# Kernel tuning notes

Measured on AMD Instinct MI355X. Metric: run time of the kernel, lower is better.

Reference implementation:

```python
import jax, jax.numpy as jnp
import numpy as np

B, S, D = 2, 2048, 768
H = 12
DK = D // H  # 64; dim_q = dim_k = dim_v
DFF = 3072
EPS = 1e-5


def layer_norm(x, w, b):
    mu = jnp.mean(x, axis=-1, keepdims=True)
    var = jnp.var(x, axis=-1, keepdims=True)
    return (x - mu) * jax.lax.rsqrt(var + EPS) * w + b


def setup_inputs() -> dict:
    key = jax.random.key(0)
    ks = jax.random.split(key, 12)
    s = 0.02
    return {
        "src": jax.random.normal(ks[0], (B, S, D), dtype=jnp.float32),
        # per-head projections stacked over heads: [H, D, DK]
        "Wq": jax.random.normal(ks[1], (H, D, DK), dtype=jnp.float32) * s,
        "bq": jnp.zeros((H, DK), dtype=jnp.float32),
        "Wk": jax.random.normal(ks[2], (H, D, DK), dtype=jnp.float32) * s,
        "bk": jnp.zeros((H, DK), dtype=jnp.float32),
        "Wv": jax.random.normal(ks[3], (H, D, DK), dtype=jnp.float32) * s,
        "bv": jnp.zeros((H, DK), dtype=jnp.float32),
        # output projection: [H*DK, D]
        "Wo": jax.random.normal(ks[4], (H * DK, D), dtype=jnp.float32) * s,
        "bo": jnp.zeros((D,), dtype=jnp.float32),
        "ln1_w": jnp.ones((D,), dtype=jnp.float32),
        "ln1_b": jnp.zeros((D,), dtype=jnp.float32),
        "W1": jax.random.normal(ks[5], (D, DFF), dtype=jnp.float32) * s,
        "b1": jnp.zeros((DFF,), dtype=jnp.float32),
        "W2": jax.random.normal(ks[6], (DFF, D), dtype=jnp.float32) * s,
        "b2": jnp.zeros((D,), dtype=jnp.float32),
        "ln2_w": jnp.ones((D,), dtype=jnp.float32),
        "ln2_b": jnp.zeros((D,), dtype=jnp.float32),
    }


def reference(src, Wq, bq, Wk, bk, Wv, bv, Wo, bo, ln1_w, ln1_b,
              W1, b1, W2, b2, ln2_w, ln2_b):
    # per-head q/k/v projections, batched over heads via einsum
    q = jnp.einsum('bsd,hdk->bhsk', src, Wq) + bq[None, :, None, :]
    k = jnp.einsum('bsd,hdk->bhsk', src, Wk) + bk[None, :, None, :]
    v = jnp.einsum('bsd,hdk->bhsk', src, Wv) + bv[None, :, None, :]
    scale = jnp.asarray(DK, src.dtype) ** 0.5
    scores = jnp.einsum('bhsk,bhtk->bhst', q, k) / scale  # [B,H,S,S]
    attn = jax.nn.softmax(scores, axis=-1)
    ctx = jnp.einsum('bhst,bhtk->bhsk', attn, v)
    # concat heads along feature dim (matches torch.cat over head outputs)
    ctx = ctx.transpose(0, 2, 1, 3).reshape(src.shape[0], src.shape[1], H * DK)
    attn_out = ctx @ Wo + bo
    x = layer_norm(src + attn_out, ln1_w, ln1_b)
    ff = jax.nn.relu(x @ W1 + b1) @ W2 + b2
    return layer_norm(x + ff, ln2_w, ln2_b)
```

## Files before the change

### kernel.cpp

```cpp
#include <hip/hip_runtime.h>
#include <hip/hip_bf16.h>

#define S_LEN 2048
#define DMODEL 768
#define NHEAD 12
#define DKH 64
#define DFF_K 3072
#define MROWS 4096
#define KSPLIT 2
#define KHALF (S_LEN / KSPLIT)

typedef __attribute__((ext_vector_type(8))) short bf16x8;
typedef __attribute__((ext_vector_type(8))) unsigned short us8;
typedef __attribute__((ext_vector_type(4))) float f32x4;

__device__ __forceinline__ float bfu2f(unsigned short u) {
  return __uint_as_float(((unsigned int)u) << 16);
}
__device__ __forceinline__ unsigned short f2bfu(float f) {
  __hip_bfloat16 h = __float2bfloat16(f);
  return *reinterpret_cast<unsigned short*>(&h);
}

__global__ __launch_bounds__(256) void convert_kernel(
    const float* __restrict__ in, unsigned short* __restrict__ out, int n4)
{
  const int i = blockIdx.x * 256 + threadIdx.x;
  if (i < n4) {
    float4 v = *(const float4*)(in + (size_t)i * 4);
    ushort4 o;
    o.x = f2bfu(v.x); o.y = f2bfu(v.y); o.z = f2bfu(v.z); o.w = f2bfu(v.w);
    *(ushort4*)(out + (size_t)i * 4) = o;
  }
}

__device__ __forceinline__ void transpose_conv_body(
    const float* in, unsigned short* out, int R, int Ctot, int head,
    int bx, int by, int tid)
{
  __shared__ float t[64][68];
  const int r0 = bx * 64;
  const int c0 = by * 64;
  const float* ib;
  int ld;
  if (head) { ib = in + (size_t)by * R * 64; ld = 64; }
  else      { ib = in + c0;                  ld = Ctot; }
  const int lr = tid >> 4;
  const int lc = (tid & 15) << 2;

#pragma unroll
  for (int rr = 0; rr < 4; ++rr) {
    const int row = rr * 16 + lr;
    float4 v = *(const float4*)(ib + (size_t)(r0 + row) * ld + lc);
    t[row][lc + 0] = v.x; t[row][lc + 1] = v.y;
    t[row][lc + 2] = v.z; t[row][lc + 3] = v.w;
  }
  __syncthreads();
#pragma unroll
  for (int rr = 0; rr < 4; ++rr) {
    const int oc = rr * 16 + lr;
    ushort4 o;
    o.x = f2bfu(t[lc + 0][oc]); o.y = f2bfu(t[lc + 1][oc]);
    o.z = f2bfu(t[lc + 2][oc]); o.w = f2bfu(t[lc + 3][oc]);
    *(ushort4*)(out + (size_t)(c0 + oc) * R + r0 + lc) = o;
  }
}

__global__ __launch_bounds__(256) void transpose_conv_kernel(
    const float* __restrict__ in, unsigned short* __restrict__ out,
    int R, int Ctot, int head)
{
  transpose_conv_body(in, out, R, Ctot, head, blockIdx.x, blockIdx.y, threadIdx.x);
}

__global__ __launch_bounds__(256) void transpose_conv4_kernel(
    const float* __restrict__ i0, const float* __restrict__ i1,
    const float* __restrict__ i2, const float* __restrict__ i3,
    unsigned short* __restrict__ o0, unsigned short* __restrict__ o1,
    unsigned short* __restrict__ o2, unsigned short* __restrict__ o3)
{
  const int z = blockIdx.z;
  const float* in = (z == 0) ? i0 : (z == 1) ? i1 : (z == 2) ? i2 : i3;
  unsigned short* out = (z == 0) ? o0 : (z == 1) ? o1 : (z == 2) ? o2 : o3;
  transpose_conv_body(in, out, DMODEL, DMODEL, (z < 3) ? 1 : 0,
                      blockIdx.x, blockIdx.y, threadIdx.x);
}

template<int BN>
__global__ __launch_bounds__(256) void mfma_gemm_kernel(
    const unsigned short* __restrict__ A,
    const unsigned short* __restrict__ BT,
    const float* __restrict__ bias,
    unsigned short* __restrict__ C,
    int K, int N, int relu, int klen, size_t out_stride)
{
  constexpr int WN = (BN == 128) ? 64 : 32;
  constexpr int NJ = WN / 16;
  __shared__ unsigned short As[128][40];
  __shared__ unsigned short Bs[BN][40];

  const int tid  = threadIdx.x;
  const int wid  = tid >> 6;
  const int lane = tid & 63;
  const int ml   = lane & 15;
  const int quad = lane >> 4;
  const int wm   = (wid & 1) * 64;
  const int wn   = (wid >> 1) * WN;
  const int row0 = blockIdx.x * 128;
  const int col0 = blockIdx.y * BN;
  const int zed  = blockIdx.z;
  const int kb0  = zed * klen;
  const int kend = kb0 + klen;

  const int sr = tid >> 2;
  const int sk = (tid & 3) << 3;

  const unsigned short* pA0 = A  + (size_t)(row0 + sr) * K + sk;
  const unsigned short* pA1 = A  + (size_t)(row0 + sr + 64) * K + sk;
  const unsigned short* pB0 = BT + (size_t)(col0 + sr) * K + sk;
  const unsigned short* pB1 = BT + (size_t)(col0 + sr + 64) * K + sk;

  f32x4 acc[4][NJ];
#pragma unroll
  for (int i = 0; i < 4; ++i)
#pragma unroll
    for (int j = 0; j < NJ; ++j)
#pragma unroll
      for (int r = 0; r < 4; ++r) acc[i][j][r] = 0.f;

  us8 ra0 = *(const us8*)(pA0 + kb0);
  us8 ra1 = *(const us8*)(pA1 + kb0);
  us8 rb0 = *(const us8*)(pB0 + kb0);
  us8 rb1;
  if (BN == 128) rb1 = *(const us8*)(pB1 + kb0);

  for (int k0 = kb0; k0 < kend; k0 += 32) {
    *(us8*)&As[sr][sk]      = ra0;
    *(us8*)&As[sr + 64][sk] = ra1;
    *(us8*)&Bs[sr][sk]      = rb0;
    if (BN == 128) *(us8*)&Bs[sr + 64][sk] = rb1;
    __syncthreads();

    const int kn = k0 + 32;
    if (kn < kend) {
      ra0 = *(const us8*)(pA0 + kn);
      ra1 = *(const us8*)(pA1 + kn);
      rb0 = *(const us8*)(pB0 + kn);
      if (BN == 128) rb1 = *(const us8*)(pB1 + kn);
    }

    bf16x8 af[4], bfr[NJ];
#pragma unroll
    for (int i = 0; i < 4; ++i)
      af[i] = *(const bf16x8*)&As[wm + i * 16 + ml][quad << 3];
#pragma unroll
    for (int j = 0; j < NJ; ++j)
      bfr[j] = *(const bf16x8*)&Bs[wn + j * 16 + ml][quad << 3];
#pragma unroll
    for (int i = 0; i < 4; ++i)
#pragma unroll
      for (int j = 0; j < NJ; ++j)
        acc[i][j] = __builtin_amdgcn_mfma_f32_16x16x32_bf16(
            af[i], bfr[j], acc[i][j], 0, 0, 0);
    __syncthreads();
  }

  unsigned short* Cz = C + (size_t)zed * out_stride;
#pragma unroll
  for (int j = 0; j < NJ; ++j) {
    const int col = col0 + wn + j * 16 + ml;
    const float bb = (zed == 0) ? bias[col] : 0.f;
#pragma unroll
    for (int i = 0; i < 4; ++i) {
      const int r0g = row0 + wm + i * 16 + (quad << 2);
#pragma unroll
      for (int r = 0; r < 4; ++r) {
        float v = acc[i][j][r] + bb;
        if (relu) v = fmaxf(v, 0.f);
        Cz[(size_t)(r0g + r) * N + col] = f2bfu(v);
      }
    }
  }
}

__global__ __launch_bounds__(256) void qkv_gemm_kernel(
    const unsigned short* __restrict__ A,
    const unsigned short* __restrict__ W0, const unsigned short* __restrict__ W1,
    const unsigned short* __restrict__ W2,
    const float* __restrict__ bq, const float* __restrict__ bk,
    const float* __restrict__ bv,
    unsigned short* __restrict__ C0, unsigned short* __restrict__ C1,
    unsigned short* __restrict__ C2)
{
  __shared__ unsigned short As[128][40];
  __shared__ unsigned short Bs[64][40];
  const int z = blockIdx.z;
  const unsigned short* BT = (z == 0) ? W0 : (z == 1) ? W1 : W2;
  const float* bias = (z == 0) ? bq : (z == 1) ? bk : bv;
  unsigned short* C = (z == 0) ? C0 : (z == 1) ? C1 : C2;
  const int K = DMODEL, N = DMODEL;

  const int tid  = threadIdx.x;
  const int wid  = tid >> 6;
  const int lane = tid & 63;
  const int ml   = lane & 15;
  const int quad = lane >> 4;
  const int wm   = (wid & 1) * 64;
  const int wn   = (wid >> 1) * 32;
  const int row0 = blockIdx.x * 128;
  const int col0 = blockIdx.y * 64;
  const int sr = tid >> 2;
  const int sk = (tid & 3) << 3;

  const unsigned short* pA0 = A  + (size_t)(row0 + sr) * K + sk;
  const unsigned short* pA1 = A  + (size_t)(row0 + sr + 64) * K + sk;
  const unsigned short* pB0 = BT + (size_t)(col0 + sr) * K + sk;

  f32x4 acc[4][2];
#pragma unroll
  for (int i = 0; i < 4; ++i)
#pragma unroll
    for (int j = 0; j < 2; ++j)
#pragma unroll
      for (int r = 0; r < 4; ++r) acc[i][j][r] = 0.f;

  us8 ra0 = *(const us8*)pA0;
  us8 ra1 = *(const us8*)pA1;
  us8 rb0 = *(const us8*)pB0;

  for (int k0 = 0; k0 < K; k0 += 32) {
    *(us8*)&As[sr][sk]      = ra0;
    *(us8*)&As[sr + 64][sk] = ra1;
    *(us8*)&Bs[sr][sk]      = rb0;
    __syncthreads();

    const int kn = k0 + 32;
    if (kn < K) {
      ra0 = *(const us8*)(pA0 + kn);
      ra1 = *(const us8*)(pA1 + kn);
      rb0 = *(const us8*)(pB0 + kn);
    }

    bf16x8 af[4], bfr[2];
#pragma unroll
    for (int i = 0; i < 4; ++i)
      af[i] = *(const bf16x8*)&As[wm + i * 16 + ml][quad << 3];
#pragma unroll
    for (int j = 0; j < 2; ++j)
      bfr[j] = *(const bf16x8*)&Bs[wn + j * 16 + ml][quad << 3];
#pragma unroll
    for (int i = 0; i < 4; ++i)
#pragma unroll
      for (int j = 0; j < 2; ++j)
        acc[i][j] = __builtin_amdgcn_mfma_f32_16x16x32_bf16(
            af[i], bfr[j], acc[i][j], 0, 0, 0);
    __syncthreads();
  }

#pragma unroll
  for (int j = 0; j < 2; ++j) {
    const int col = col0 + wn + j * 16 + ml;
    const float bb = bias[col];
#pragma unroll
    for (int i = 0; i < 4; ++i) {
      const int r0g = row0 + wm + i * 16 + (quad << 2);
      if (z == 2) {
        const int bb_ = r0g >> 11, s = r0g & 2047;
        const int hh = col >> 6, dd = col & 63;
        ushort4 o;
        o.x = f2bfu(acc[i][j][0] + bb); o.y = f2bfu(acc[i][j][1] + bb);
        o.z = f2bfu(acc[i][j][2] + bb); o.w = f2bfu(acc[i][j][3] + bb);
        *(ushort4*)(C + ((size_t)((bb_ * NHEAD + hh) * DKH + dd)) * S_LEN + s) = o;
      } else {
#pragma unroll
        for (int r = 0; r < 4; ++r)
          C[(size_t)(r0g + r) * N + col] = f2bfu(acc[i][j][r] + bb);
      }
    }
  }
}

#define SCL2E 0.1803368822f
__global__ __launch_bounds__(256, 3) void flash_attn_mfma(
    const unsigned short* __restrict__ Q,
    const unsigned short* __restrict__ K,
    const unsigned short* __restrict__ VT,
    float* __restrict__ Opart,
    float* __restrict__ Lpart)
{
  __shared__ unsigned short Ks[64][64];
  __shared__ unsigned short Vs[64][64];
  __shared__ unsigned short QP[4][2][16][64];

  const int tid  = threadIdx.x;
  const int wid  = tid >> 6;
  const int lane = tid & 63;
  const int ml   = lane & 15;
  const int quad = lane >> 4;
  const int h    = blockIdx.x, b = blockIdx.y;
  const int q0   = (blockIdx.z >> 1) * 128;
  const int ks   = blockIdx.z & 1;
  const int kt0  = ks * KHALF;

  const size_t qkbase = ((size_t)b * S_LEN) * DMODEL + (size_t)h * DKH;
  const size_t vtbase = ((size_t)(b * NHEAD + h)) * DKH * S_LEN;

  const int sr  = tid >> 2;
  const int scb = (tid & 3) << 5;
  const int ssw = (sr & 7) << 4;
  const int fsw = (ml & 7) << 4;

  char* ksrow = (char*)&Ks[sr][0];
  char* vsrow = (char*)&Vs[sr][0];

  const int qrA = q0 + wid * 32 + ml;
  const int qrB = qrA + 16;
  const unsigned short* qpg = Q + qkbase;
  bf16x8 qfA0 = *(const bf16x8*)(qpg + (size_t)qrA * DMODEL + (quad << 3));
  bf16x8 qfA1 = *(const bf16x8*)(qpg + (size_t)qrA * DMODEL + 32 + (quad << 3));
  bf16x8 qfB0 = *(const bf16x8*)(qpg + (size_t)qrB * DMODEL + (quad << 3));
  bf16x8 qfB1 = *(const bf16x8*)(qpg + (size_t)qrB * DMODEL + 32 + (quad << 3));

  const unsigned short* pK = K + qkbase + (size_t)(kt0 + sr) * DMODEL + (scb >> 1);
  const unsigned short* pV = VT + vtbase + (size_t)sr * S_LEN + kt0 + (scb >> 1);

  float lsumA = 0.f, lsumB = 0.f;
  f32x4 oaccA[4], oaccB[4];
#pragma unroll
  for (int dt = 0; dt < 4; ++dt)
#pragma unroll
    for (int r = 0; r < 4; ++r) { oaccA[dt][r] = 0.f; oaccB[dt][r] = 0.f; }

  us8 rk0 = *(const us8*)(pK);
  us8 rk1 = *(const us8*)(pK + 8);
  us8 rv0 = *(const us8*)(pV);
  us8 rv1 = *(const us8*)(pV + 8);

  char* qpA = (char*)&QP[wid][0][ml][0];
  char* qpB = (char*)&QP[wid][1][ml][0];

  for (int kt = 0; kt < KHALF; kt += 64) {
    __syncthreads();
    *(us8*)(ksrow + ((scb +  0) ^ ssw)) = rk0;
    *(us8*)(ksrow + ((scb + 16) ^ ssw)) = rk1;
    *(us8*)(vsrow + ((scb +  0) ^ ssw)) = rv0;
    *(us8*)(vsrow + ((scb + 16) ^ ssw)) = rv1;
    __syncthreads();

    const int ktn = kt + 64;
    if (ktn < KHALF) {
      rk0 = *(const us8*)(pK + (size_t)ktn * DMODEL);
      rk1 = *(const us8*)(pK + (size_t)ktn * DMODEL + 8);
      rv0 = *(const us8*)(pV + ktn);
      rv1 = *(const us8*)(pV + ktn + 8);
    }

    f32x4 sA[4], sB[4];
#pragma unroll
    for (int mt = 0; mt < 4; ++mt)
#pragma unroll
      for (int r = 0; r < 4; ++r) { sA[mt][r] = 0.f; sB[mt][r] = 0.f; }
#pragma unroll
    for (int mt = 0; mt < 4; ++mt) {
      char* kr = (char*)&Ks[mt * 16 + ml][0];
      bf16x8 kf0 = *(const bf16x8*)(kr + (((quad << 4) +  0) ^ fsw));
      bf16x8 kf1 = *(const bf16x8*)(kr + (((quad << 4) + 64) ^ fsw));
      sA[mt] = __builtin_amdgcn_mfma_f32_16x16x32_bf16(kf0, qfA0, sA[mt], 0, 0, 0);
      sA[mt] = __builtin_amdgcn_mfma_f32_16x16x32_bf16(kf1, qfA1, sA[mt], 0, 0, 0);
      sB[mt] = __builtin_amdgcn_mfma_f32_16x16x32_bf16(kf0, qfB0, sB[mt], 0, 0, 0);
      sB[mt] = __builtin_amdgcn_mfma_f32_16x16x32_bf16(kf1, qfB1, sB[mt], 0, 0, 0);
    }

#pragma unroll
    for (int mt = 0; mt < 4; ++mt) {
      float e0 = exp2f(sA[mt][0] * SCL2E), e1 = exp2f(sA[mt][1] * SCL2E),
            e2 = exp2f(sA[mt][2] * SCL2E), e3 = exp2f(sA[mt][3] * SCL2E);
      lsumA += (e0 + e1) + (e2 + e3);
      ushort4 oA;
      oA.x = f2bfu(e0); oA.y = f2bfu(e1); oA.z = f2bfu(e2); oA.w = f2bfu(e3);
      *(ushort4*)(qpA + (((mt << 5) + (quad << 3)) ^ fsw)) = oA;
      e0 = exp2f(sB[mt][0] * SCL2E); e1 = exp2f(sB[mt][1] * SCL2E);
      e2 = exp2f(sB[mt][2] * SCL2E); e3 = exp2f(sB[mt][3] * SCL2E);
      lsumB += (e0 + e1) + (e2 + e3);
      ushort4 oB;
      oB.x = f2bfu(e0); oB.y = f2bfu(e1); oB.z = f2bfu(e2); oB.w = f2bfu(e3);
      *(ushort4*)(qpB + (((mt << 5) + (quad << 3)) ^ fsw)) = oB;
    }
    bf16x8 pfA0 = *(const bf16x8*)(qpA + (((quad << 4) +  0) ^ fsw));
    bf16x8 pfA1 = *(const bf16x8*)(qpA + (((quad << 4) + 64) ^ fsw));
    bf16x8 pfB0 = *(const bf16x8*)(qpB + (((quad << 4) +  0) ^ fsw));
    bf16x8 pfB1 = *(const bf16x8*)(qpB + (((quad << 4) + 64) ^ fsw));

#pragma unroll
    for (int dt = 0; dt < 4; ++dt) {
      char* vr = (char*)&Vs[dt * 16 + ml][0];
      bf16x8 vf0 = *(const bf16x8*)(vr + (((quad << 4) +  0) ^ fsw));
      bf16x8 vf1 = *(const bf16x8*)(vr + (((quad << 4) + 64) ^ fsw));
      oaccA[dt] = __builtin_amdgcn_mfma_f32_16x16x32_bf16(vf0, pfA0, oaccA[dt], 0, 0, 0);
      oaccA[dt] = __builtin_amdgcn_mfma_f32_16x16x32_bf16(vf1, pfA1, oaccA[dt], 0, 0, 0);
      oaccB[dt] = __builtin_amdgcn_mfma_f32_16x16x32_bf16(vf0, pfB0, oaccB[dt], 0, 0, 0);
      oaccB[dt] = __builtin_amdgcn_mfma_f32_16x16x32_bf16(vf1, pfB1, oaccB[dt], 0, 0, 0);
    }
  }

  lsumA += __shfl_xor(lsumA, 16);
  lsumA += __shfl_xor(lsumA, 32);
  lsumB += __shfl_xor(lsumB, 16);
  lsumB += __shfl_xor(lsumB, 32);
  const size_t lbase = (((size_t)(ks * 2 + b)) * NHEAD + h) * S_LEN;
  const size_t obaseA = (lbase + qrA) * DKH;
  const size_t obaseB = (lbase + qrB) * DKH;
#pragma unroll
  for (int dt = 0; dt < 4; ++dt) {
    *(f32x4*)&Opart[obaseA + dt * 16 + (quad << 2)] = oaccA[dt];
    *(f32x4*)&Opart[obaseB + dt * 16 + (quad << 2)] = oaccB[dt];
  }
  if (quad == 0) {
    Lpart[lbase + qrA] = lsumA;
    Lpart[lbase + qrB] = lsumB;
  }
}

__global__ __launch_bounds__(256) void attn_combine_kernel(
    const float* __restrict__ Op,
    const float* __restrict__ Lp,
    unsigned short* __restrict__ O)
{
  const int s = blockIdx.x & (S_LEN - 1);
  const int b = blockIdx.x >> 11;
  const int tid = threadIdx.x;
  const size_t ohalf = (size_t)2 * NHEAD * S_LEN * DKH;
  const size_t lhalf = (size_t)2 * NHEAD * S_LEN;
#pragma unroll
  for (int c = tid; c < DMODEL; c += 256) {
    const int hh = c >> 6, dd = c & 63;
    const size_t li = ((size_t)b * NHEAD + hh) * S_LEN + s;
    const size_t oi = li * DKH + dd;
    const float o = Op[oi] + Op[ohalf + oi];
    const float l = Lp[li] + Lp[lhalf + li];
    O[((size_t)b * S_LEN + s) * DMODEL + c] = f2bfu(o / l);
  }
}

__global__ __launch_bounds__(256) void add_ln_kernel(
    const void* __restrict__ X, const void* __restrict__ Y,
    const void* __restrict__ Y2,
    const float* __restrict__ w, const float* __restrict__ bvec,
    void* __restrict__ out, int xbf, int ybf, int obf)
{
  __shared__ float buf[DMODEL];
  __shared__ float rbuf[8];
  const int tid  = threadIdx.x;
  const int lane = tid & 63, wv = tid >> 6;
  const size_t base = (size_t)blockIdx.x * DMODEL;

  float s = 0.f, s2 = 0.f;
#pragma unroll
  for (int j = tid; j < DMODEL; j += 256) {
    float xv = xbf ? bfu2f(((const unsigned short*)X)[base + j])
                   : ((const float*)X)[base + j];
    float yv = ybf ? bfu2f(((const unsigned short*)Y)[base + j])
                   : ((const float*)Y)[base + j];
    float v = xv + yv;
    if (Y2) v += ybf ? bfu2f(((const unsigned short*)Y2)[base + j])
                     : ((const float*)Y2)[base + j];
    buf[j] = v; s += v; s2 += v * v;
  }
#pragma unroll
  for (int o = 32; o; o >>= 1) { s += __shfl_xor(s, o); s2 += __shfl_xor(s2, o); }
  if (lane == 0) { rbuf[wv] = s; rbuf[4 + wv] = s2; }
  __syncthreads();
  const float S  = rbuf[0] + rbuf[1] + rbuf[2] + rbuf[3];
  const float S2 = rbuf[4] + rbuf[5] + rbuf[6] + rbuf[7];
  const float mean = S * (1.f / (float)DMODEL);
  const float var  = S2 * (1.f / (float)DMODEL) - mean * mean;
  const float rstd = rsqrtf(var + 1e-5f);
#pragma unroll
  for (int j = tid; j < DMODEL; j += 256) {
    float v = (buf[j] - mean) * rstd * w[j] + bvec[j];
    if (obf) ((unsigned short*)out)[base + j] = f2bfu(v);
    else     ((float*)out)[base + j] = v;
  }
}

extern "C" void kernel_launch(void* const* d_in, const int* in_sizes, int n_in,
                              void* d_out, int out_size, void* d_ws, size_t ws_size,
                              hipStream_t stream) {
  const float* src  = (const float*)d_in[0];
  const float* Wq   = (const float*)d_in[1];
  const float* bq   = (const float*)d_in[2];
  const float* Wk   = (const float*)d_in[3];
  const float* bk   = (const float*)d_in[4];
  const float* Wv   = (const float*)d_in[5];
  const float* bv   = (const float*)d_in[6];
  const float* Wo   = (const float*)d_in[7];
  const float* bo   = (const float*)d_in[8];
  const float* ln1w = (const float*)d_in[9];
  const float* ln1b = (const float*)d_in[10];
  const float* W1   = (const float*)d_in[11];
  const float* b1   = (const float*)d_in[12];
  const float* W2   = (const float*)d_in[13];
  const float* b2   = (const float*)d_in[14];
  const float* ln2w = (const float*)d_in[15];
  const float* ln2b = (const float*)d_in[16];
  (void)ws_size; (void)in_sizes; (void)n_in; (void)out_size;

  unsigned short* p = (unsigned short*)d_ws;
  const size_t SEG = (size_t)MROWS * DMODEL;
  unsigned short* srcb = p; p += SEG;
  unsigned short* qb   = p; p += SEG;
  unsigned short* kb_  = p; p += SEG;
  unsigned short* vbT  = p; p += SEG;
  unsigned short* ctx  = p; p += SEG;
  unsigned short* ff   = p; p += (size_t)MROWS * DFF_K;
  unsigned short* wqt  = p; p += (size_t)DMODEL * DMODEL;
  unsigned short* wkt  = p; p += (size_t)DMODEL * DMODEL;
  unsigned short* wvt  = p; p += (size_t)DMODEL * DMODEL;
  unsigned short* wot  = p; p += (size_t)DMODEL * DMODEL;
  unsigned short* w1t  = p; p += (size_t)DMODEL * DFF_K;
  unsigned short* w2t  = p; p += (size_t)DMODEL * DFF_K;
  unsigned short* x1 = kb_;
  float* opart = (float*)ff;
  float* lpart = (float*)wqt;

  dim3 blk(256);

  convert_kernel<<<dim3(SEG / 1024), blk, 0, stream>>>(src, srcb, (int)(SEG / 4));
  transpose_conv4_kernel<<<dim3(12, 12, 4), blk, 0, stream>>>(
      Wq, Wk, Wv, Wo, wqt, wkt, wvt, wot);
  transpose_conv_kernel<<<dim3(12, 48), blk, 0, stream>>>(W1, w1t, DMODEL, DFF_K, 0);
  transpose_conv_kernel<<<dim3(48, 12), blk, 0, stream>>>(W2, w2t, DFF_K, DMODEL, 0);

  dim3 gqkv(MROWS / 128, DMODEL / 64, 3);
  qkv_gemm_kernel<<<gqkv, blk, 0, stream>>>(srcb, wqt, wkt, wvt, bq, bk, bv,
                                            qb, kb_, vbT);

  dim3 ga(NHEAD, 2, (S_LEN / 128) * KSPLIT);
  flash_attn_mfma<<<ga, blk, 0, stream>>>(qb, kb_, vbT, opart, lpart);
  attn_combine_kernel<<<dim3(MROWS), blk, 0, stream>>>(opart, lpart, ctx);

  dim3 gWo(MROWS / 128, DMODEL / 64, 2);
  mfma_gemm_kernel<64><<<gWo, blk, 0, stream>>>(ctx, wot, bo, qb,
                                                DMODEL, DMODEL, 0, DMODEL / 2, 2 * SEG);

  add_ln_kernel<<<dim3(MROWS), blk, 0, stream>>>(srcb, qb, vbT,
                                                 ln1w, ln1b, x1, 1, 1, 1);

  dim3 gF1(MROWS / 128, DFF_K / 128, 1);
  mfma_gemm_kernel<128><<<gF1, blk, 0, stream>>>(x1, w1t, b1, ff,
                                                 DMODEL, DFF_K, 1, DMODEL, 0);

  dim3 gW2(MROWS / 128, DMODEL / 64, 2);
  mfma_gemm_kernel<64><<<gW2, blk, 0, stream>>>(ff, w2t, b2, qb,
                                                DFF_K, DMODEL, 0, DFF_K / 2, 2 * SEG);

  add_ln_kernel<<<dim3(MROWS), blk, 0, stream>>>(x1, qb, vbT,
                                                 ln2w, ln2b, (float*)d_out, 1, 1, 0);
}
```

Baseline: 299.3 us.

## Use direct global-to-LDS async loads with double-buffered swizzled tiles in GEMMs

Replaces the register-staged global loads and LDS stores in the generic and QKV GEMM kernels with global_load_lds async copies into a double-buffered, XOR-swizzled LDS layout. The K step grows from 32 to 64, halving the number of barriers per tile, and the next tile's copy overlaps the MFMA work on the current one. LDS use per block roughly triples, which may lower occupancy. The swizzle is meant to avoid bank conflicts without the padding used before.

```diff
diff --git a/kernel.cpp b/kernel.cpp
--- a/kernel.cpp
+++ b/kernel.cpp
@@ -20,6 +20,12 @@
 __device__ __forceinline__ unsigned short f2bfu(float f) {
   __hip_bfloat16 h = __float2bfloat16(f);
   return *reinterpret_cast<unsigned short*>(&h);
+}
+
+__device__ __forceinline__ void async16(const unsigned short* g, unsigned short* l) {
+  __builtin_amdgcn_global_load_lds(
+      (const __attribute__((address_space(1))) unsigned int*)g,
+      (__attribute__((address_space(3))) unsigned int*)l, 16, 0, 0);
 }
 
 __global__ __launch_bounds__(256) void convert_kernel(
@@ -87,6 +93,29 @@
 }
 
 template<int BN>
+__device__ __forceinline__ void stage_tile(
+    const unsigned short* __restrict__ Ab,
+    const unsigned short* __restrict__ Bb,
+    unsigned short* As, unsigned short* Bs,
+    int wid, int lane, int K, int kofs)
+{
+  const int r = lane >> 3;
+  const int s = lane & 7;
+#pragma unroll
+  for (int p = 0; p < 4; ++p) {
+    const int row = wid * 32 + p * 8 + r;
+    async16(Ab + (size_t)row * K + kofs + ((s ^ (row & 7)) << 3),
+            As + (size_t)(wid * 32 + p * 8) * 64);
+  }
+#pragma unroll
+  for (int p = 0; p < BN / 32; ++p) {
+    const int row = wid * (BN / 4) + p * 8 + r;
+    async16(Bb + (size_t)row * K + kofs + ((s ^ (row & 7)) << 3),
+            Bs + (size_t)(wid * (BN / 4) + p * 8) * 64);
+  }
+}
+
+template<int BN>
 __global__ __launch_bounds__(256) void mfma_gemm_kernel(
     const unsigned short* __restrict__ A,
     const unsigned short* __restrict__ BT,
@@ -96,8 +125,8 @@
 {
   constexpr int WN = (BN == 128) ? 64 : 32;
   constexpr int NJ = WN / 16;
-  __shared__ unsigned short As[128][40];
-  __shared__ unsigned short Bs[BN][40];
+  __shared__ unsigned short As[2][128][64];
+  __shared__ unsigned short Bs[2][BN][64];
 
   const int tid  = threadIdx.x;
   const int wid  = tid >> 6;
@@ -110,15 +139,11 @@
   const int col0 = blockIdx.y * BN;
   const int zed  = blockIdx.z;
   const int kb0  = zed * klen;
-  const int kend = kb0 + klen;
-
-  const int sr = tid >> 2;
-  const int sk = (tid & 3) << 3;
-
-  const unsigned short* pA0 = A  + (size_t)(row0 + sr) * K + sk;
-  const unsigned short* pA1 = A  + (size_t)(row0 + sr + 64) * K + sk;
-  const unsigned short* pB0 = BT + (size_t)(col0 + sr) * K + sk;
-  const unsigned short* pB1 = BT + (size_t)(col0 + sr + 64) * K + sk;
+  const int nsteps = klen >> 6;
+  const int fsw = (ml & 7) << 4;
+
+  const unsigned short* Ab = A  + (size_t)row0 * K + kb0;
+  const unsigned short* Bb = BT + (size_t)col0 * K + kb0;
 
   f32x4 acc[4][NJ];
 #pragma unroll
@@ -128,40 +153,37 @@
 #pragma unroll
       for (int r = 0; r < 4; ++r) acc[i][j][r] = 0.f;
 
-  us8 ra0 = *(const us8*)(pA0 + kb0);
-  us8 ra1 = *(const us8*)(pA1 + kb0);
-  us8 rb0 = *(const us8*)(pB0 + kb0);
-  us8 rb1;
-  if (BN == 128) rb1 = *(const us8*)(pB1 + kb0);
-
-  for (int k0 = kb0; k0 < kend; k0 += 32) {
-    *(us8*)&As[sr][sk]      = ra0;
-    *(us8*)&As[sr + 64][sk] = ra1;
-    *(us8*)&Bs[sr][sk]      = rb0;
-    if (BN == 128) *(us8*)&Bs[sr + 64][sk] = rb1;
-    __syncthreads();
-
-    const int kn = k0 + 32;
-    if (kn < kend) {
-      ra0 = *(const us8*)(pA0 + kn);
-      ra1 = *(const us8*)(pA1 + kn);
-      rb0 = *(const us8*)(pB0 + kn);
-      if (BN == 128) rb1 = *(const us8*)(pB1 + kn);
-    }
-
-    bf16x8 af[4], bfr[NJ];
-#pragma unroll
-    for (int i = 0; i < 4; ++i)
-      af[i] = *(const bf16x8*)&As[wm + i * 16 + ml][quad << 3];
-#pragma unroll
-    for (int j = 0; j < NJ; ++j)
-      bfr[j] = *(const bf16x8*)&Bs[wn + j * 16 + ml][quad << 3];
-#pragma unroll
-    for (int i = 0; i < 4; ++i)
-#pragma unroll
-      for (int j = 0; j < NJ; ++j)
-        acc[i][j] = __builtin_amdgcn_mfma_f32_16x16x32_bf16(
-            af[i], bfr[j], acc[i][j], 0, 0, 0);
+  stage_tile<BN>(Ab, Bb, &As[0][0][0], &Bs[0][0][0], wid, lane, K, 0);
+  __syncthreads();
+
+  for (int st = 0; st < nsteps; ++st) {
+    const int cur = st & 1;
+    if (st + 1 < nsteps)
+      stage_tile<BN>(Ab, Bb, &As[cur ^ 1][0][0], &Bs[cur ^ 1][0][0],
+                     wid, lane, K, (st + 1) << 6);
+
+    const char* Ac = (const char*)&As[cur][0][0];
+    const char* Bc = (const char*)&Bs[cur][0][0];
+#pragma unroll
+    for (int h = 0; h < 2; ++h) {
+      bf16x8 af[4], bfr[NJ];
+#pragma unroll
+      for (int i = 0; i < 4; ++i) {
+        const int ar = wm + i * 16 + ml;
+        af[i] = *(const bf16x8*)(Ac + ar * 128 + (((h << 6) + (quad << 4)) ^ fsw));
+      }
+#pragma unroll
+      for (int j = 0; j < NJ; ++j) {
+        const int br = wn + j * 16 + ml;
+        bfr[j] = *(const bf16x8*)(Bc + br * 128 + (((h << 6) + (quad << 4)) ^ fsw));
+      }
+#pragma unroll
+      for (int i = 0; i < 4; ++i)
+#pragma unroll
+        for (int j = 0; j < NJ; ++j)
+          acc[i][j] = __builtin_amdgcn_mfma_f32_16x16x32_bf16(
+              af[i], bfr[j], acc[i][j], 0, 0, 0);
+    }
     __syncthreads();
   }
 
@@ -192,8 +214,8 @@
     unsigned short* __restrict__ C0, unsigned short* __restrict__ C1,
     unsigned short* __restrict__ C2)
 {
-  __shared__ unsigned short As[128][40];
-  __shared__ unsigned short Bs[64][40];
+  __shared__ unsigned short As[2][128][64];
+  __shared__ unsigned short Bs[2][64][64];
   const int z = blockIdx.z;
   const unsigned short* BT = (z == 0) ? W0 : (z == 1) ? W1 : W2;
   const float* bias = (z == 0) ? bq : (z == 1) ? bk : bv;
@@ -209,12 +231,10 @@
   const int wn   = (wid >> 1) * 32;
   const int row0 = blockIdx.x * 128;
   const int col0 = blockIdx.y * 64;
-  const int sr = tid >> 2;
-  const int sk = (tid & 3) << 3;
-
-  const unsigned short* pA0 = A  + (size_t)(row0 + sr) * K + sk;
-  const unsigned short* pA1 = A  + (size_t)(row0 + sr + 64) * K + sk;
-  const unsigned short* pB0 = BT + (size_t)(col0 + sr) * K + sk;
+  const int fsw = (ml & 7) << 4;
+
+  const unsigned short* Ab = A  + (size_t)row0 * K;
+  const unsigned short* Bb = BT + (size_t)col0 * K;
 
   f32x4 acc[4][2];
 #pragma unroll
@@ -224,36 +244,38 @@
 #pragma unroll
       for (int r = 0; r < 4; ++r) acc[i][j][r] = 0.f;
 
-  us8 ra0 = *(const us8*)pA0;
-  us8 ra1 = *(const us8*)pA1;
-  us8 rb0 = *(const us8*)pB0;
-
-  for (int k0 = 0; k0 < K; k0 += 32) {
-    *(us8*)&As[sr][sk]      = ra0;
-    *(us8*)&As[sr + 64][sk] = ra1;
-    *(us8*)&Bs[sr][sk]      = rb0;
-    __syncthreads();
-
-    const int kn = k0 + 32;
-    if (kn < K) {
-      ra0 = *(const us8*)(pA0 + kn);
-      ra1 = *(const us8*)(pA1 + kn);
-      rb0 = *(const us8*)(pB0 + kn);
-    }
-
-    bf16x8 af[4], bfr[2];
-#pragma unroll
-    for (int i = 0; i < 4; ++i)
-      af[i] = *(const bf16x8*)&As[wm + i * 16 + ml][quad << 3];
-#pragma unroll
-    for (int j = 0; j < 2; ++j)
-      bfr[j] = *(const bf16x8*)&Bs[wn + j * 16 + ml][quad << 3];
-#pragma unroll
-    for (int i = 0; i < 4; ++i)
-#pragma unroll
-      for (int j = 0; j < 2; ++j)
-        acc[i][j] = __builtin_amdgcn_mfma_f32_16x16x32_bf16(
-            af[i], bfr[j], acc[i][j], 0, 0, 0);
+  stage_tile<64>(Ab, Bb, &As[0][0][0], &Bs[0][0][0], wid, lane, K, 0);
+  __syncthreads();
+
+  const int nsteps = K >> 6;
+  for (int st = 0; st < nsteps; ++st) {
+    const int cur = st & 1;
+    if (st + 1 < nsteps)
+      stage_tile<64>(Ab, Bb, &As[cur ^ 1][0][0], &Bs[cur ^ 1][0][0],
+                     wid, lane, K, (st + 1) << 6);
+
+    const char* Ac = (const char*)&As[cur][0][0];
+    const char* Bc = (const char*)&Bs[cur][0][0];
+#pragma unroll
+    for (int h = 0; h < 2; ++h) {
+      bf16x8 af[4], bfr[2];
+#pragma unroll
+      for (int i = 0; i < 4; ++i) {
+        const int ar = wm + i * 16 + ml;
+        af[i] = *(const bf16x8*)(Ac + ar * 128 + (((h << 6) + (quad << 4)) ^ fsw));
+      }
+#pragma unroll
+      for (int j = 0; j < 2; ++j) {
+        const int br = wn + j * 16 + ml;
+        bfr[j] = *(const bf16x8*)(Bc + br * 128 + (((h << 6) + (quad << 4)) ^ fsw));
+      }
+#pragma unroll
+      for (int i = 0; i < 4; ++i)
+#pragma unroll
+        for (int j = 0; j < 2; ++j)
+          acc[i][j] = __builtin_amdgcn_mfma_f32_16x16x32_bf16(
+              af[i], bfr[j], acc[i][j], 0, 0, 0);
+    }
     __syncthreads();
   }
 
```

After: 287.6 us. 1.04x faster.
